# Kernel tuning notes

Hardware: AMD Instinct MI355X
Metric: run time of the kernel (lower is better)

The kernel has to match this reference:

```python
import jax, jax.numpy as jnp
import numpy as np
from jax import lax

V, B, C, H, W, D, G_DEF = 5, 2, 32, 128, 160, 32, 8


def _combine(proj):
    # proj: [B,2,4,4]; [:,0]=extrinsic, [:,1]=intrinsic; new[:, :3, :4] = K[:3,:3] @ E[:3,:4]
    ext, K = proj[:, 0], proj[:, 1]
    top = jnp.einsum('bij,bjk->bik', K[:, :3, :3], ext[:, :3, :4])
    return ext.at[:, :3, :4].set(top)


def _bilinear(img, x, y):
    # img [C,H,W]; x,y [N] pixel coords; zeros padding, align_corners=True (torch grid_sample)
    Ch, Hh, Wh = img.shape
    x0 = jnp.floor(x); y0 = jnp.floor(y)
    wx1 = x - x0; wy1 = y - y0
    def gather(xi, yi):
        valid = ((xi >= 0) & (xi <= Wh - 1) & (yi >= 0) & (yi <= Hh - 1)).astype(img.dtype)
        xc = jnp.clip(xi, 0, Wh - 1).astype(jnp.int32)
        yc = jnp.clip(yi, 0, Hh - 1).astype(jnp.int32)
        return img[:, yc, xc] * valid
    return (gather(x0, y0) * ((1 - wx1) * (1 - wy1)) + gather(x0 + 1, y0) * (wx1 * (1 - wy1))
            + gather(x0, y0 + 1) * ((1 - wx1) * wy1) + gather(x0 + 1, y0 + 1) * (wx1 * wy1))


def _conv3d(x, w, b, pad):
    y = lax.conv_general_dilated(x, w, (1, 1, 1), [(pad, pad)] * 3,
                                 dimension_numbers=('NCDHW', 'OIDHW', 'NCDHW'))
    return y + b[None, :, None, None, None]


def setup_inputs():
    key = jax.random.key(0)
    ks = jax.random.split(key, 8)
    features = jax.random.normal(ks[0], (V, B, C, H, W), jnp.float32)
    pm = np.zeros((B, V, 2, 4, 4), np.float32)
    for v in range(V):
        E = np.eye(4, dtype=np.float32); E[0, 3] = 0.05 * v  # small baseline along x
        K = np.eye(4, dtype=np.float32)
        K[0, 0] = K[1, 1] = float(W); K[0, 2] = W / 2.0; K[1, 2] = H / 2.0
        pm[:, v, 0] = E; pm[:, v, 1] = K
    proj_matrices = jnp.asarray(pm)
    d = jnp.linspace(1.0, 3.0, D, dtype=jnp.float32)
    depth_values = jnp.broadcast_to(d[None, :, None, None], (B, D, H, W))
    s = 0.1
    reg_w1 = jax.random.normal(ks[1], (8, G_DEF, 3, 3, 3), jnp.float32) * s
    reg_b1 = jnp.zeros((8,), jnp.float32)
    reg_w2 = jax.random.normal(ks[2], (1, 8, 3, 3, 3), jnp.float32) * s
    reg_b2 = jnp.zeros((1,), jnp.float32)
    pw_w1 = jax.random.normal(ks[3], (16, 1, 1, 1, 1), jnp.float32) * s
    pw_b1 = jnp.zeros((16,), jnp.float32)
    pw_w2 = jax.random.normal(ks[4], (8, 16, 1, 1, 1), jnp.float32) * s
    pw_b2 = jnp.zeros((8,), jnp.float32)
    pw_w3 = jax.random.normal(ks[5], (1, 8, 1, 1, 1), jnp.float32) * s
    pw_b3 = jnp.zeros((1,), jnp.float32)
    return dict(features=features, proj_matrices=proj_matrices, depth_values=depth_values,
                reg_w1=reg_w1, reg_b1=reg_b1, reg_w2=reg_w2, reg_b2=reg_b2,
                pw_w1=pw_w1, pw_b1=pw_b1, pw_w2=pw_w2, pw_b2=pw_b2,
                pw_w3=pw_w3, pw_b3=pw_b3, num_depth=D, G=G_DEF)


def reference(features, proj_matrices, depth_values, reg_w1, reg_b1, reg_w2, reg_b2,
              pw_w1, pw_b1, pw_w2, pw_b2, pw_w3, pw_b3, num_depth, G):
    Vn, Bn, Cn, Hn, Wn = features.shape
    Dn = num_depth
    ref_fea = features[0].reshape(Bn, G, Cn // G, Hn, Wn)
    ref_proj = _combine(proj_matrices[:, 0])
    ref_proj_inv = jnp.linalg.inv(ref_proj)
    ys, xs = jnp.meshgrid(jnp.arange(Hn, dtype=jnp.float32), jnp.arange(Wn, dtype=jnp.float32), indexing='ij')
    xyz = jnp.stack([xs.ravel(), ys.ravel(), jnp.ones(Hn * Wn, jnp.float32)], 0)  # [3, HW]
    sim_sum = 0.0; w_sum = 0.0; vws = []
    for v in range(1, Vn):  # fixed small view loop
        proj = jnp.einsum('bij,bjk->bik', _combine(proj_matrices[:, v]), ref_proj_inv)
        rot_xyz = jnp.einsum('bij,jn->bin', proj[:, :3, :3], xyz)  # [B,3,HW]
        pxyz = rot_xyz[:, :, None, :] * depth_values.reshape(Bn, 1, Dn, Hn * Wn) \
               + proj[:, :3, 3][:, :, None, None]  # [B,3,D,HW]
        # grid is computed under no_grad in torch -> stop_gradient
        x = lax.stop_gradient((pxyz[:, 0] / pxyz[:, 2]).reshape(Bn, -1))
        y = lax.stop_gradient((pxyz[:, 1] / pxyz[:, 2]).reshape(Bn, -1))
        warped = jax.vmap(_bilinear)(features[v], x, y).reshape(Bn, G, Cn // G, Dn, Hn, Wn)
        sim = (warped * ref_fea[:, :, :, None]).mean(2)  # [B,G,D,H,W] group correlation
        p = jax.nn.softmax(lax.stop_gradient(sim), axis=1)  # detached in torch
        ent = -(p * jnp.log(p + 1e-7)).sum(1, keepdims=True)  # [B,1,D,H,W]
        h = jax.nn.relu(_conv3d(ent, pw_w1, pw_b1, 0))
        h = jax.nn.relu(_conv3d(h, pw_w2, pw_b2, 0))
        vw = jax.nn.sigmoid(_conv3d(h, pw_w3, pw_b3, 0)).max(axis=2)  # [B,1,H,W]
        vws.append(vw)
        sim_sum = sim_sum + sim * vw[:, None]  # broadcast [B,1,1,H,W]
        w_sum = w_sum + vw[:, None]
    view_weights = jnp.concatenate(vws, axis=1)  # [B,V-1,H,W]
    similarity = sim_sum / (w_sum + 1e-6)
    h = jax.nn.relu(_conv3d(similarity, reg_w1, reg_b1, 1))
    prob_volume_pre = _conv3d(h, reg_w2, reg_b2, 1)[:, 0]  # [B,D,H,W]
    prob_volume = jax.nn.softmax(prob_volume_pre, axis=1)
    depth = (prob_volume * depth_values).sum(1)  # [B,H,W]
    pv = lax.stop_gradient(prob_volume)
    padded = jnp.pad(pv, ((0, 0), (1, 2), (0, 0), (0, 0)))
    # 4 * avg_pool3d(kernel=(4,1,1)) == sliding window sum over depth
    sum4 = lax.reduce_window(padded, 0.0, lax.add, (1, 4, 1, 1), (1, 1, 1, 1), 'VALID')
    didx = jnp.clip((pv * jnp.arange(Dn, dtype=pv.dtype)[None, :, None, None]).sum(1).astype(jnp.int32), 0, Dn - 1)
    photometric_confidence = jnp.take_along_axis(sum4, didx[:, None], axis=1)[:, 0]
    return depth, photometric_confidence, view_weights, prob_volume_pre, similarity
```

## Files before the change

kernel.cpp:

```cpp
#include <hip/hip_runtime.h>
#include <hip/hip_bf16.h>
#include <hip/hip_fp16.h>

#define V_  5
#define B_  2
#define C_  32
#define H_  128
#define W_  160
#define D_  32
#define G_  8
#define HW_  (H_*W_)
#define DHW_ (D_*HW_)

#define LOG2E_ 1.4426950408889634f
#define LN2_   0.6931471805599453f
#define LN8_   2.0794415416798357f

typedef _Float16 h8 __attribute__((ext_vector_type(8)));
typedef _Float16 h4 __attribute__((ext_vector_type(4)));
typedef _Float16 h2 __attribute__((ext_vector_type(2)));
typedef float    f4 __attribute__((ext_vector_type(4)));

__device__ inline float fdot2f(h2 a, h2 b, float c) {
#if __has_builtin(__builtin_amdgcn_fdot2)
    return __builtin_amdgcn_fdot2(a, b, c, false);
#else
    return fmaf((float)a[0], (float)b[0], fmaf((float)a[1], (float)b[1], c));
#endif
}



__device__ inline void combine_mat(const float* m, float out[4][4]) {
    const float* ext = m;
    const float* K   = m + 16;
    for (int r = 0; r < 4; ++r)
        for (int c = 0; c < 4; ++c)
            out[r][c] = ext[r*4 + c];
    for (int r = 0; r < 3; ++r)
        for (int c = 0; c < 4; ++c) {
            float s = 0.f;
            for (int k = 0; k < 3; ++k) s += K[r*4 + k] * ext[k*4 + c];
            out[r][c] = s;
        }
}

__device__ inline void invert4(const float Ain[4][4], float Inv[4][4]) {
    float A[4][4];
    for (int r = 0; r < 4; ++r)
        for (int c = 0; c < 4; ++c) {
            A[r][c]   = Ain[r][c];
            Inv[r][c] = (r == c) ? 1.f : 0.f;
        }
    for (int k = 0; k < 4; ++k) {
        int p = k; float best = fabsf(A[k][k]);
        for (int r = k + 1; r < 4; ++r) {
            float v = fabsf(A[r][k]);
            if (v > best) { best = v; p = r; }
        }
        if (p != k) {
            for (int j = 0; j < 4; ++j) {
                float t = A[k][j]; A[k][j] = A[p][j]; A[p][j] = t;
                t = Inv[k][j]; Inv[k][j] = Inv[p][j]; Inv[p][j] = t;
            }
        }
        float dinv = 1.f / A[k][k];
        for (int j = 0; j < 4; ++j) { A[k][j] *= dinv; Inv[k][j] *= dinv; }
        for (int r = 0; r < 4; ++r) {
            if (r == k) continue;
            float f = A[r][k];
            for (int j = 0; j < 4; ++j) {
                A[r][j]  -= f * A[k][j];
                Inv[r][j] -= f * Inv[k][j];
            }
        }
    }
}

__global__ __launch_bounds__(1024) void k_proj(
    const float* __restrict__ pm,
    const float* __restrict__ pw_w1, const float* __restrict__ pw_b1,
    const float* __restrict__ pw_w2, const float* __restrict__ pw_b2,
    const float* __restrict__ pw_w3, const float* __restrict__ pw_b3,
    const float* __restrict__ reg_w1, const float* __restrict__ reg_w2,
    float* __restrict__ proj_ws, float* __restrict__ tabw,
    _Float16* __restrict__ wh1, _Float16* __restrict__ wh2)
{
    int tid = threadIdx.x;
    if (tid < B_) {
        int b = tid;
        float C0[4][4], C0inv[4][4];
        combine_mat(pm + (b * V_ + 0) * 32, C0);
        invert4(C0, C0inv);
        for (int v = 1; v < V_; ++v) {
            float Cv[4][4];
            combine_mat(pm + (b * V_ + v) * 32, Cv);
            float* o = proj_ws + (b * 4 + (v - 1)) * 12;
            for (int r = 0; r < 3; ++r)
                for (int c = 0; c < 4; ++c) {
                    float s = 0.f;
                    for (int k = 0; k < 4; ++k) s += Cv[r][k] * C0inv[k][c];
                    o[r*4 + c] = s;
                }
        }
    }
    for (int i = tid; i < 36*16*8; i += 1024) {
        int ic = i & 7; int m = (i >> 3) & 15; int slot = i >> 7;
        int wx = slot & 3; int grp = slot >> 2;
        wh1[i] = (_Float16)((wx < 3 && m < 8) ? reg_w1[(m*8 + ic)*27 + grp*3 + wx] : 0.f);
    }
    for (int i = tid; i < 36*8; i += 1024) {
        int ic = i & 7; int slot = i >> 3;
        int wx = slot & 3; int grp = slot >> 2;
        wh2[i] = (_Float16)((wx < 3) ? reg_w2[ic*27 + grp*3 + wx] : 0.f);
    }
    float ent = (float)tid * (LN8_ / 1023.0f);
    float h2v[8];
    #pragma unroll
    for (int j = 0; j < 8; ++j) h2v[j] = pw_b2[j];
    for (int k = 0; k < 16; ++k) {
        float h1 = fmaxf(ent * pw_w1[k] + pw_b1[k], 0.f);
        #pragma unroll
        for (int j = 0; j < 8; ++j) h2v[j] += pw_w2[j*16 + k] * h1;
    }
    float o3 = pw_b3[0];
    #pragma unroll
    for (int j = 0; j < 8; ++j) o3 += pw_w3[j] * fmaxf(h2v[j], 0.f);
    tabw[tid] = 1.f / (1.f + expf(-o3));
}

__global__ __launch_bounds__(1024) void k_transpose(
    const float* __restrict__ in, _Float16* __restrict__ out)
{
    __shared__ float s[32][33];
    const int tx = threadIdx.x, ty = threadIdx.y;
    const int tid = ty * 32 + tx;
    const int hw0 = blockIdx.x * 32;
    const int vb  = blockIdx.y;
    s[ty][tx] = in[(vb * 32 + ty) * HW_ + hw0 + tx];
    __syncthreads();
    if (tid < 256) {
        int hw = tid >> 3, q = tid & 7;
        h4 hv;
        #pragma unroll
        for (int i = 0; i < 4; ++i) hv[i] = (_Float16)s[q*4 + i][hw];
        *(h4*)(out + ((size_t)vb * HW_ + hw0 + hw) * 32 + q*4) = hv;
    }
}

__global__ __launch_bounds__(1024) void k_main(
    const _Float16* __restrict__ featT,
    const float* __restrict__ depthv,
    const float* __restrict__ proj_ws,
    const float* __restrict__ tabw,
    float* __restrict__ out_vw,
    float* __restrict__ out_sim,
    _Float16* __restrict__ simh)
{
    const int tid = threadIdx.x;
    const int wv   = tid >> 6;
    const int lane = tid & 63;
    const int j    = lane >> 5;
    const int d    = lane & 31;
    const int pxl  = wv * 2 + j;
    const int w0 = blockIdx.x * 32;
    const int h  = blockIdx.y;
    const int b  = blockIdx.z;
    const int w  = w0 + pxl;
    const int p  = h * W_ + w;

    __shared__ float tab_s[1024];
    __shared__ float proj_s[48];
    __shared__ float s_sim[G_][32][33];

    tab_s[tid] = tabw[tid];
    if (tid < 48) proj_s[tid] = proj_ws[b * 48 + tid];
    __syncthreads();

    const h8* rp = (const h8*)(featT + ((size_t)b * HW_ + p) * 32);
    h8 r8[4];
    #pragma unroll
    for (int cc = 0; cc < 4; ++cc) r8[cc] = rp[cc];

    const float depth = depthv[(b * D_ + d) * HW_ + p];
    const float xf = (float)w, yf = (float)h;

    float simsum[G_];
    #pragma unroll
    for (int g = 0; g < G_; ++g) simsum[g] = 0.f;
    float wsum = 0.f;

    for (int v = 1; v < V_; ++v) {
        const float* P = &proj_s[(v - 1) * 12];
        float px = (P[0]*xf + P[1]*yf + P[2])  * depth + P[3];
        float py = (P[4]*xf + P[5]*yf + P[6])  * depth + P[7];
        float pz = (P[8]*xf + P[9]*yf + P[10]) * depth + P[11];
        float rz = __builtin_amdgcn_rcpf(pz);
        float xs = px * rz;
        float ys = py * rz;

        float xr = rintf(xs);
        float yr = rintf(ys);
        xs = (fabsf(xs - xr) < 1e-4f) ? xr : xs;
        ys = (fabsf(ys - yr) < 1e-4f) ? yr : ys;

        float x0 = floorf(xs), y0 = floorf(ys);
        float wx1 = xs - x0,  wy1 = ys - y0;
        float wx0 = 1.f - wx1, wy0 = 1.f - wy1;

        bool vx0 = (x0 >= 0.f)     && (x0 <= (float)(W_-1));
        bool vx1 = (x0+1.f >= 0.f) && (x0+1.f <= (float)(W_-1));
        bool vy0 = (y0 >= 0.f)     && (y0 <= (float)(H_-1));
        bool vy1 = (y0+1.f >= 0.f) && (y0+1.f <= (float)(H_-1));

        int xc0 = (int)fminf(fmaxf(x0,     0.f), (float)(W_-1));
        int xc1 = (int)fminf(fmaxf(x0+1.f, 0.f), (float)(W_-1));
        int yc0 = (int)fminf(fmaxf(y0,     0.f), (float)(H_-1));
        int yc1 = (int)fminf(fmaxf(y0+1.f, 0.f), (float)(H_-1));

        float w00 = (vx0 && vy0) ? (wx0 * wy0) : 0.f;
        float w01 = (vx1 && vy0) ? (wx1 * wy0) : 0.f;
        float w10 = (vx0 && vy1) ? (wx0 * wy1) : 0.f;
        float w11 = (vx1 && vy1) ? (wx1 * wy1) : 0.f;

        const _Float16* vbp = featT + (size_t)(v * B_ + b) * HW_ * 32;

        float sim[G_];
        #pragma unroll
        for (int g = 0; g < G_; ++g) sim[g] = 0.f;

        bool top = __any(w00 > 0.f || w01 > 0.f);
        bool bot = __any(w10 > 0.f || w11 > 0.f);

        if (top) {
            h2 w00h = { (_Float16)w00, (_Float16)w00 };
            h2 w01h = { (_Float16)w01, (_Float16)w01 };
            const h8* t00 = (const h8*)(vbp + (size_t)(yc0 * W_ + xc0) * 32);
            const h8* t01 = (const h8*)(vbp + (size_t)(yc0 * W_ + xc1) * 32);
            #pragma unroll
            for (int cc = 0; cc < 4; ++cc) {
                h8 a = t00[cc], bb = t01[cc];
                const h2* ap = (const h2*)&a;
                const h2* bp = (const h2*)&bb;
                const h2* rv2 = (const h2*)&r8[cc];
                #pragma unroll
                for (int jp = 0; jp < 4; ++jp) {
                    h2 fv = ap[jp] * w00h + bp[jp] * w01h;
                    int g = cc*2 + (jp >> 1);
                    sim[g] = fdot2f(fv, rv2[jp], sim[g]);
                }
            }
        }
        if (bot) {
            h2 w10h = { (_Float16)w10, (_Float16)w10 };
            h2 w11h = { (_Float16)w11, (_Float16)w11 };
            const h8* t10 = (const h8*)(vbp + (size_t)(yc1 * W_ + xc0) * 32);
            const h8* t11 = (const h8*)(vbp + (size_t)(yc1 * W_ + xc1) * 32);
            #pragma unroll
            for (int cc = 0; cc < 4; ++cc) {
                h8 cq = t10[cc], dq = t11[cc];
                const h2* cp = (const h2*)&cq;
                const h2* dp = (const h2*)&dq;
                const h2* rv2 = (const h2*)&r8[cc];
                #pragma unroll
                for (int jp = 0; jp < 4; ++jp) {
                    h2 fv = cp[jp] * w10h + dp[jp] * w11h;
                    int g = cc*2 + (jp >> 1);
                    sim[g] = fdot2f(fv, rv2[jp], sim[g]);
                }
            }
        }

        #pragma unroll
        for (int g = 0; g < G_; ++g) sim[g] *= 0.25f;

        float m = sim[0];
        #pragma unroll
        for (int g = 1; g < G_; ++g) m = fmaxf(m, sim[g]);
        float es = 0.f, edot = 0.f;
        #pragma unroll
        for (int g = 0; g < G_; ++g) {
            float e = exp2f((sim[g] - m) * LOG2E_);
            es += e;
            edot = fmaf(e, sim[g], edot);
        }
        float inv_es = __builtin_amdgcn_rcpf(es);
        float ent = m + log2f(es) * LN2_ - edot * inv_es;

        float t = ent * (1023.0f / LN8_);
        t = fminf(fmaxf(t, 0.f), 1022.999f);
        int it = (int)t;
        float fr = t - (float)it;
        float lo = tab_s[it], hi = tab_s[it + 1];
        float sig = fmaf(hi - lo, fr, lo);

        float mv = sig;
        #pragma unroll
        for (int k = 16; k >= 1; k >>= 1)
            mv = fmaxf(mv, __shfl_xor(mv, k, 64));
        if (d == 0)
            out_vw[(b * 4 + (v - 1)) * HW_ + p] = mv;

        #pragma unroll
        for (int g = 0; g < G_; ++g) simsum[g] = fmaf(sim[g], mv, simsum[g]);
        wsum += mv;
    }

    float wn = __builtin_amdgcn_rcpf(wsum + 1e-6f);
    #pragma unroll
    for (int g = 0; g < G_; ++g) s_sim[g][d][pxl] = simsum[g] * wn;
    __syncthreads();

    const int tx = tid & 31;
    const int ty = tid >> 5;
    float* so = out_sim + (size_t)b * G_ * DHW_ + ty * HW_ + h * W_ + w0 + tx;
    h8 hv;
    #pragma unroll
    for (int g = 0; g < G_; ++g) {
        float val = s_sim[g][ty][tx];
        so[(size_t)g * DHW_] = val;
        hv[g] = (_Float16)val;
    }
    *(h8*)(simh + ((size_t)(b * D_ + ty) * HW_ + h * W_ + w0 + tx) * 8) = hv;
}


__global__ __launch_bounds__(256) void k_conv1m(
    const _Float16* __restrict__ in,
    const _Float16* __restrict__ wh,
    const float* __restrict__ bias,
    _Float16* __restrict__ outh)
{
    __shared__ _Float16 halo[6*10*34*8 + 8];
    const int tid = threadIdx.x;
    const int w0 = blockIdx.x * 32;
    const int h0 = blockIdx.y * 8;
    const int z  = blockIdx.z;
    const int b  = z >> 3;
    const int d0 = (z & 7) * 4;

    for (int pos = tid; pos < 2040; pos += 256) {
        int wx = pos % 34; int r = pos / 34; int hy = r % 10; int dz = r / 10;
        int gw = w0 + wx - 1, gh = h0 + hy - 1, gd = d0 + dz - 1;
        uint4 val = make_uint4(0u, 0u, 0u, 0u);
        if (gw >= 0 && gw < W_ && gh >= 0 && gh < H_ && gd >= 0 && gd < D_)
            val = *(const uint4*)(in + (((size_t)(b*D_ + gd)*H_ + gh)*W_ + gw)*8);
        *(uint4*)(halo + pos*8) = val;
    }
    if (tid == 0) *(uint4*)(halo + 6*10*34*8) = make_uint4(0u, 0u, 0u, 0u);

    const int wave = tid >> 6, lane = tid & 63;
    const int n = lane & 15, q = lane >> 4;

    h8 afrag[9];
    #pragma unroll
    for (int grp = 0; grp < 9; ++grp)
        afrag[grp] = *(const h8*)(wh + ((grp*4 + q)*16 + n)*8);

    f4 binit;
    #pragma unroll
    for (int reg = 0; reg < 4; ++reg)
        binit[reg] = (q < 2) ? bias[q*4 + reg] : 0.f;

    __syncthreads();

    const int lane_off = (n + q) * 16;

    #pragma unroll
    for (int it = 0; it < 4; ++it) {
        int t = wave*4 + it;
        int h_row = t >> 1, whalf = t & 1;
        const char* base = (const char*)halo + h_row*544 + whalf*256 + lane_off;
        #pragma unroll
        for (int dout = 0; dout < 4; ++dout) {
            f4 acc = binit;
            #pragma unroll
            for (int dz = 0; dz < 3; ++dz) {
                #pragma unroll
                for (int hy = 0; hy < 3; ++hy) {
                    h8 bfrag = *(const h8*)(base + (((dout + dz)*10 + hy)*544));
                    acc = __builtin_amdgcn_mfma_f32_16x16x32_f16(afrag[dz*3 + hy], bfrag, acc, 0, 0, 0);
                }
            }
            if (q < 2) {
                h4 hv;
                #pragma unroll
                for (int reg = 0; reg < 4; ++reg) hv[reg] = (_Float16)fmaxf(acc[reg], 0.f);
                *(h4*)(outh + (((size_t)(b*D_ + d0 + dout)*H_ + h0 + h_row)*W_ + w0 + whalf*16 + n)*8 + q*4) = hv;
            }
        }
    }
}

__global__ __launch_bounds__(256) void k_conv2m(
    const _Float16* __restrict__ in,
    const _Float16* __restrict__ wh,
    const float* __restrict__ bias,
    float* __restrict__ out)
{
    __shared__ _Float16 halo[6*10*34*8 + 8];
    const int tid = threadIdx.x;
    const int w0 = blockIdx.x * 32;
    const int h0 = blockIdx.y * 8;
    const int z  = blockIdx.z;
    const int b  = z >> 3;
    const int d0 = (z & 7) * 4;

    for (int pos = tid; pos < 2040; pos += 256) {
        int wx = pos % 34; int r = pos / 34; int hy = r % 10; int dz = r / 10;
        int gw = w0 + wx - 1, gh = h0 + hy - 1, gd = d0 + dz - 1;
        uint4 val = make_uint4(0u, 0u, 0u, 0u);
        if (gw >= 0 && gw < W_ && gh >= 0 && gh < H_ && gd >= 0 && gd < D_)
            val = *(const uint4*)(in + (((size_t)(b*D_ + gd)*H_ + gh)*W_ + gw)*8);
        *(uint4*)(halo + pos*8) = val;
    }
    if (tid == 0) *(uint4*)(halo + 6*10*34*8) = make_uint4(0u, 0u, 0u, 0u);

    const int wave = tid >> 6, lane = tid & 63;
    const int n = lane & 15, q = lane >> 4;

    h8 afrag[9];
    #pragma unroll
    for (int grp = 0; grp < 9; ++grp) {
        h8 a;
        #pragma unroll
        for (int e = 0; e < 8; ++e) a[e] = (_Float16)0.f;
        if (n == 0) a = *(const h8*)(wh + (grp*4 + q)*8);
        afrag[grp] = a;
    }
    const float b0 = bias[0];

    __syncthreads();

    const int lane_off = (n + q) * 16;

    #pragma unroll
    for (int it = 0; it < 4; ++it) {
        int t = wave*4 + it;
        int h_row = t >> 1, whalf = t & 1;
        const char* base = (const char*)halo + h_row*544 + whalf*256 + lane_off;
        #pragma unroll
        for (int dout = 0; dout < 4; ++dout) {
            f4 acc;
            acc[0] = (q == 0) ? b0 : 0.f;
            acc[1] = 0.f; acc[2] = 0.f; acc[3] = 0.f;
            #pragma unroll
            for (int dz = 0; dz < 3; ++dz) {
                #pragma unroll
                for (int hy = 0; hy < 3; ++hy) {
                    h8 bfrag = *(const h8*)(base + (((dout + dz)*10 + hy)*544));
                    acc = __builtin_amdgcn_mfma_f32_16x16x32_f16(afrag[dz*3 + hy], bfrag, acc, 0, 0, 0);
                }
            }
            if (q == 0)
                out[(((size_t)(b*D_ + d0 + dout)*H_ + h0 + h_row)*W_ + w0 + whalf*16 + n)] = acc[0];
        }
    }
}

__global__ __launch_bounds__(256) void k_final(
    const float* __restrict__ pvp,
    const float* __restrict__ depthv,
    float* __restrict__ out_depth,
    float* __restrict__ out_conf)
{
    int i = blockIdx.x * 256 + threadIdx.x;
    if (i >= B_ * HW_) return;
    int b = i / HW_;
    int p = i - b * HW_;

    const float* pp = pvp + b * DHW_ + p;
    const float* dv = depthv + b * DHW_ + p;

    float x[D_];
    float m = -3.4e38f;
    #pragma unroll
    for (int d = 0; d < D_; ++d) { x[d] = pp[d * HW_]; m = fmaxf(m, x[d]); }
    float s = 0.f;
    #pragma unroll
    for (int d = 0; d < D_; ++d) { x[d] = exp2f((x[d] - m) * LOG2E_); s += x[d]; }
    float inv = 1.f / s;

    float dep = 0.f, fd = 0.f;
    #pragma unroll
    for (int d = 0; d < D_; ++d) {
        float pv = x[d] * inv;
        x[d] = pv;
        dep = fmaf(pv, dv[d * HW_], dep);
        fd  = fmaf(pv, (float)d, fd);
    }
    int di = (int)fd;
    di = di < 0 ? 0 : (di > D_ - 1 ? D_ - 1 : di);
    float conf = 0.f;
    #pragma unroll
    for (int k = 0; k < 4; ++k) {
        int idx = di - 1 + k;
        if (idx >= 0 && idx < D_) conf += x[idx];
    }
    out_depth[i] = dep;
    out_conf[i]  = conf;
}

extern "C" void kernel_launch(void* const* d_in, const int* in_sizes, int n_in,
                              void* d_out, int out_size, void* d_ws, size_t ws_size,
                              hipStream_t stream) {
    const float* feat   = (const float*)d_in[0];
    const float* pm     = (const float*)d_in[1];
    const float* depthv = (const float*)d_in[2];
    const float* reg_w1 = (const float*)d_in[3];
    const float* reg_b1 = (const float*)d_in[4];
    const float* reg_w2 = (const float*)d_in[5];
    const float* reg_b2 = (const float*)d_in[6];
    const float* pw_w1  = (const float*)d_in[7];
    const float* pw_b1  = (const float*)d_in[8];
    const float* pw_w2  = (const float*)d_in[9];
    const float* pw_b2  = (const float*)d_in[10];
    const float* pw_w3  = (const float*)d_in[11];
    const float* pw_b3  = (const float*)d_in[12];

    float* out = (float*)d_out;
    float* out_depth = out;
    float* out_conf  = out + B_*HW_;
    float* out_vw    = out + 2*B_*HW_;
    float* out_pvp   = out_vw + B_*4*HW_;
    float* out_sim   = out_pvp + B_*DHW_;

    float* ws      = (float*)d_ws;
    float* proj_ws = ws;
    float* tabw    = ws + 128;
    _Float16* wh1  = (_Float16*)(ws + 1152);
    _Float16* wh2  = (_Float16*)(ws + 3456);
    _Float16* featT = (_Float16*)(ws + 4736);
    _Float16* hidh  = (_Float16*)(ws + 4736);
    _Float16* simh  = (_Float16*)(ws + 4736 + 5242880);

    hipLaunchKernelGGL(k_proj, dim3(1), dim3(1024), 0, stream,
                       pm, pw_w1, pw_b1, pw_w2, pw_b2, pw_w3, pw_b3,
                       reg_w1, reg_w2, proj_ws, tabw, wh1, wh2);

    hipLaunchKernelGGL(k_transpose, dim3(HW_/32, V_*B_), dim3(32, 32), 0, stream,
                       feat, featT);

    hipLaunchKernelGGL(k_main, dim3(W_/32, H_, B_), dim3(1024), 0, stream,
                       featT, depthv, proj_ws, tabw, out_vw, out_sim, simh);

    hipLaunchKernelGGL(k_conv1m, dim3(W_/32, H_/8, B_*D_/4), dim3(256), 0, stream,
                       simh, wh1, reg_b1, hidh);

    hipLaunchKernelGGL(k_conv2m, dim3(W_/32, H_/8, B_*D_/4), dim3(256), 0, stream,
                       hidh, wh2, reg_b2, out_pvp);

    hipLaunchKernelGGL(k_final, dim3((B_*HW_ + 255)/256), dim3(256), 0, stream,
                       out_pvp, depthv, out_depth, out_conf);
}
```

Measured before the change: 209.3 us.

## Software-pipeline view gathers in k_main and halve block size

Unrolls the loop over source views into a two-stage software pipeline. The top-row bilinear taps for the next view are fetched into registers while the current view's similarity, entropy and weight are computed, which is meant to hide gather latency. The block also shrinks from 1024 to 512 threads (16 pixels per block), with launch bounds asking for 4 blocks per CU, to raise occupancy and scheduling flexibility. In exchange, holding two views' prefetched fp16 taps raises register pressure and could cause spills.

```diff
diff --git a/kernel.cpp b/kernel.cpp
--- a/kernel.cpp
+++ b/kernel.cpp
@@ -148,7 +148,117 @@
     }
 }
 
-__global__ __launch_bounds__(1024) void k_main(
+
+#define VPREP(S, VV) do { \
+    const float* P = &proj_s[((VV) - 1) * 12]; \
+    float px_ = (P[0]*xf + P[1]*yf + P[2])  * depth + P[3]; \
+    float py_ = (P[4]*xf + P[5]*yf + P[6])  * depth + P[7]; \
+    float pz_ = (P[8]*xf + P[9]*yf + P[10]) * depth + P[11]; \
+    float rz = __builtin_amdgcn_rcpf(pz_); \
+    float xs = px_ * rz, ys = py_ * rz; \
+    float xr = rintf(xs), yr = rintf(ys); \
+    xs = (fabsf(xs - xr) < 1e-4f) ? xr : xs; \
+    ys = (fabsf(ys - yr) < 1e-4f) ? yr : ys; \
+    float x0 = floorf(xs), y0 = floorf(ys); \
+    float wx1 = xs - x0, wy1 = ys - y0; \
+    float wx0 = 1.f - wx1, wy0 = 1.f - wy1; \
+    bool vx0 = (x0 >= 0.f)     && (x0 <= (float)(W_-1)); \
+    bool vx1 = (x0+1.f >= 0.f) && (x0+1.f <= (float)(W_-1)); \
+    bool vy0 = (y0 >= 0.f)     && (y0 <= (float)(H_-1)); \
+    bool vy1 = (y0+1.f >= 0.f) && (y0+1.f <= (float)(H_-1)); \
+    int xc0 = (int)fminf(fmaxf(x0,     0.f), (float)(W_-1)); \
+    int xc1 = (int)fminf(fmaxf(x0+1.f, 0.f), (float)(W_-1)); \
+    int yc0 = (int)fminf(fmaxf(y0,     0.f), (float)(H_-1)); \
+    int yc1 = (int)fminf(fmaxf(y0+1.f, 0.f), (float)(H_-1)); \
+    w00##S = (vx0 && vy0) ? (wx0 * wy0) : 0.f; \
+    w01##S = (vx1 && vy0) ? (wx1 * wy0) : 0.f; \
+    w10##S = (vx0 && vy1) ? (wx0 * wy1) : 0.f; \
+    w11##S = (vx1 && vy1) ? (wx1 * wy1) : 0.f; \
+    o10##S = (uint32_t)(yc1 * W_ + xc0); \
+    o11##S = (uint32_t)(yc1 * W_ + xc1); \
+    top##S = __any(w00##S > 0.f || w01##S > 0.f); \
+    bot##S = __any(w10##S > 0.f || w11##S > 0.f); \
+    if (top##S) { \
+        const _Float16* vbp = featT + (size_t)((VV) * B_ + b) * HW_ * 32; \
+        const h8* t00 = (const h8*)(vbp + (size_t)(yc0 * W_ + xc0) * 32); \
+        const h8* t01 = (const h8*)(vbp + (size_t)(yc0 * W_ + xc1) * 32); \
+        _Pragma("unroll") \
+        for (int cc = 0; cc < 4; ++cc) { a##S[cc] = t00[cc]; b##S[cc] = t01[cc]; } \
+    } \
+} while (0)
+
+#define VCONSUME(S, VV) do { \
+    float sim[G_]; \
+    _Pragma("unroll") \
+    for (int g = 0; g < G_; ++g) sim[g] = 0.f; \
+    if (top##S) { \
+        h2 w00h = { (_Float16)w00##S, (_Float16)w00##S }; \
+        h2 w01h = { (_Float16)w01##S, (_Float16)w01##S }; \
+        _Pragma("unroll") \
+        for (int cc = 0; cc < 4; ++cc) { \
+            const h2* ap = (const h2*)&a##S[cc]; \
+            const h2* bp = (const h2*)&b##S[cc]; \
+            const h2* rv2 = (const h2*)&r8[cc]; \
+            _Pragma("unroll") \
+            for (int jp = 0; jp < 4; ++jp) { \
+                h2 fv = ap[jp] * w00h + bp[jp] * w01h; \
+                int g = cc*2 + (jp >> 1); \
+                sim[g] = fdot2f(fv, rv2[jp], sim[g]); \
+            } \
+        } \
+    } \
+    if (bot##S) { \
+        const _Float16* vbp = featT + (size_t)((VV) * B_ + b) * HW_ * 32; \
+        const h8* t10 = (const h8*)(vbp + (size_t)o10##S * 32); \
+        const h8* t11 = (const h8*)(vbp + (size_t)o11##S * 32); \
+        h2 w10h = { (_Float16)w10##S, (_Float16)w10##S }; \
+        h2 w11h = { (_Float16)w11##S, (_Float16)w11##S }; \
+        _Pragma("unroll") \
+        for (int cc = 0; cc < 4; ++cc) { \
+            h8 cq = t10[cc], dq = t11[cc]; \
+            const h2* cp = (const h2*)&cq; \
+            const h2* dp = (const h2*)&dq; \
+            const h2* rv2 = (const h2*)&r8[cc]; \
+            _Pragma("unroll") \
+            for (int jp = 0; jp < 4; ++jp) { \
+                h2 fv = cp[jp] * w10h + dp[jp] * w11h; \
+                int g = cc*2 + (jp >> 1); \
+                sim[g] = fdot2f(fv, rv2[jp], sim[g]); \
+            } \
+        } \
+    } \
+    _Pragma("unroll") \
+    for (int g = 0; g < G_; ++g) sim[g] *= 0.25f; \
+    float m = sim[0]; \
+    _Pragma("unroll") \
+    for (int g = 1; g < G_; ++g) m = fmaxf(m, sim[g]); \
+    float es = 0.f, edot = 0.f; \
+    _Pragma("unroll") \
+    for (int g = 0; g < G_; ++g) { \
+        float e = exp2f((sim[g] - m) * LOG2E_); \
+        es += e; \
+        edot = fmaf(e, sim[g], edot); \
+    } \
+    float inv_es = __builtin_amdgcn_rcpf(es); \
+    float ent = m + log2f(es) * LN2_ - edot * inv_es; \
+    float t = ent * (1023.0f / LN8_); \
+    t = fminf(fmaxf(t, 0.f), 1022.999f); \
+    int it = (int)t; \
+    float fr = t - (float)it; \
+    float lo = tab_s[it], hi = tab_s[it + 1]; \
+    float sig = fmaf(hi - lo, fr, lo); \
+    float mv = sig; \
+    _Pragma("unroll") \
+    for (int k = 16; k >= 1; k >>= 1) \
+        mv = fmaxf(mv, __shfl_xor(mv, k, 64)); \
+    if (d == 0) \
+        out_vw[(b * 4 + ((VV) - 1)) * HW_ + p] = mv; \
+    _Pragma("unroll") \
+    for (int g = 0; g < G_; ++g) simsum[g] = fmaf(sim[g], mv, simsum[g]); \
+    wsum += mv; \
+} while (0)
+
+__global__ __launch_bounds__(512, 4) void k_main(
     const _Float16* __restrict__ featT,
     const float* __restrict__ depthv,
     const float* __restrict__ proj_ws,
@@ -163,7 +273,7 @@
     const int j    = lane >> 5;
     const int d    = lane & 31;
     const int pxl  = wv * 2 + j;
-    const int w0 = blockIdx.x * 32;
+    const int w0 = blockIdx.x * 16;
     const int h  = blockIdx.y;
     const int b  = blockIdx.z;
     const int w  = w0 + pxl;
@@ -171,9 +281,9 @@
 
     __shared__ float tab_s[1024];
     __shared__ float proj_s[48];
-    __shared__ float s_sim[G_][32][33];
-
-    tab_s[tid] = tabw[tid];
+    __shared__ float s_sim[G_][32][17];
+
+    for (int i = tid; i < 1024; i += 512) tab_s[i] = tabw[i];
     if (tid < 48) proj_s[tid] = proj_ws[b * 48 + tid];
     __syncthreads();
 
@@ -190,129 +300,27 @@
     for (int g = 0; g < G_; ++g) simsum[g] = 0.f;
     float wsum = 0.f;
 
-    for (int v = 1; v < V_; ++v) {
-        const float* P = &proj_s[(v - 1) * 12];
-        float px = (P[0]*xf + P[1]*yf + P[2])  * depth + P[3];
-        float py = (P[4]*xf + P[5]*yf + P[6])  * depth + P[7];
-        float pz = (P[8]*xf + P[9]*yf + P[10]) * depth + P[11];
-        float rz = __builtin_amdgcn_rcpf(pz);
-        float xs = px * rz;
-        float ys = py * rz;
-
-        float xr = rintf(xs);
-        float yr = rintf(ys);
-        xs = (fabsf(xs - xr) < 1e-4f) ? xr : xs;
-        ys = (fabsf(ys - yr) < 1e-4f) ? yr : ys;
-
-        float x0 = floorf(xs), y0 = floorf(ys);
-        float wx1 = xs - x0,  wy1 = ys - y0;
-        float wx0 = 1.f - wx1, wy0 = 1.f - wy1;
-
-        bool vx0 = (x0 >= 0.f)     && (x0 <= (float)(W_-1));
-        bool vx1 = (x0+1.f >= 0.f) && (x0+1.f <= (float)(W_-1));
-        bool vy0 = (y0 >= 0.f)     && (y0 <= (float)(H_-1));
-        bool vy1 = (y0+1.f >= 0.f) && (y0+1.f <= (float)(H_-1));
-
-        int xc0 = (int)fminf(fmaxf(x0,     0.f), (float)(W_-1));
-        int xc1 = (int)fminf(fmaxf(x0+1.f, 0.f), (float)(W_-1));
-        int yc0 = (int)fminf(fmaxf(y0,     0.f), (float)(H_-1));
-        int yc1 = (int)fminf(fmaxf(y0+1.f, 0.f), (float)(H_-1));
-
-        float w00 = (vx0 && vy0) ? (wx0 * wy0) : 0.f;
-        float w01 = (vx1 && vy0) ? (wx1 * wy0) : 0.f;
-        float w10 = (vx0 && vy1) ? (wx0 * wy1) : 0.f;
-        float w11 = (vx1 && vy1) ? (wx1 * wy1) : 0.f;
-
-        const _Float16* vbp = featT + (size_t)(v * B_ + b) * HW_ * 32;
-
-        float sim[G_];
-        #pragma unroll
-        for (int g = 0; g < G_; ++g) sim[g] = 0.f;
-
-        bool top = __any(w00 > 0.f || w01 > 0.f);
-        bool bot = __any(w10 > 0.f || w11 > 0.f);
-
-        if (top) {
-            h2 w00h = { (_Float16)w00, (_Float16)w00 };
-            h2 w01h = { (_Float16)w01, (_Float16)w01 };
-            const h8* t00 = (const h8*)(vbp + (size_t)(yc0 * W_ + xc0) * 32);
-            const h8* t01 = (const h8*)(vbp + (size_t)(yc0 * W_ + xc1) * 32);
-            #pragma unroll
-            for (int cc = 0; cc < 4; ++cc) {
-                h8 a = t00[cc], bb = t01[cc];
-                const h2* ap = (const h2*)&a;
-                const h2* bp = (const h2*)&bb;
-                const h2* rv2 = (const h2*)&r8[cc];
-                #pragma unroll
-                for (int jp = 0; jp < 4; ++jp) {
-                    h2 fv = ap[jp] * w00h + bp[jp] * w01h;
-                    int g = cc*2 + (jp >> 1);
-                    sim[g] = fdot2f(fv, rv2[jp], sim[g]);
-                }
-            }
-        }
-        if (bot) {
-            h2 w10h = { (_Float16)w10, (_Float16)w10 };
-            h2 w11h = { (_Float16)w11, (_Float16)w11 };
-            const h8* t10 = (const h8*)(vbp + (size_t)(yc1 * W_ + xc0) * 32);
-            const h8* t11 = (const h8*)(vbp + (size_t)(yc1 * W_ + xc1) * 32);
-            #pragma unroll
-            for (int cc = 0; cc < 4; ++cc) {
-                h8 cq = t10[cc], dq = t11[cc];
-                const h2* cp = (const h2*)&cq;
-                const h2* dp = (const h2*)&dq;
-                const h2* rv2 = (const h2*)&r8[cc];
-                #pragma unroll
-                for (int jp = 0; jp < 4; ++jp) {
-                    h2 fv = cp[jp] * w10h + dp[jp] * w11h;
-                    int g = cc*2 + (jp >> 1);
-                    sim[g] = fdot2f(fv, rv2[jp], sim[g]);
-                }
-            }
-        }
-
-        #pragma unroll
-        for (int g = 0; g < G_; ++g) sim[g] *= 0.25f;
-
-        float m = sim[0];
-        #pragma unroll
-        for (int g = 1; g < G_; ++g) m = fmaxf(m, sim[g]);
-        float es = 0.f, edot = 0.f;
-        #pragma unroll
-        for (int g = 0; g < G_; ++g) {
-            float e = exp2f((sim[g] - m) * LOG2E_);
-            es += e;
-            edot = fmaf(e, sim[g], edot);
-        }
-        float inv_es = __builtin_amdgcn_rcpf(es);
-        float ent = m + log2f(es) * LN2_ - edot * inv_es;
-
-        float t = ent * (1023.0f / LN8_);
-        t = fminf(fmaxf(t, 0.f), 1022.999f);
-        int it = (int)t;
-        float fr = t - (float)it;
-        float lo = tab_s[it], hi = tab_s[it + 1];
-        float sig = fmaf(hi - lo, fr, lo);
-
-        float mv = sig;
-        #pragma unroll
-        for (int k = 16; k >= 1; k >>= 1)
-            mv = fmaxf(mv, __shfl_xor(mv, k, 64));
-        if (d == 0)
-            out_vw[(b * 4 + (v - 1)) * HW_ + p] = mv;
-
-        #pragma unroll
-        for (int g = 0; g < G_; ++g) simsum[g] = fmaf(sim[g], mv, simsum[g]);
-        wsum += mv;
-    }
+    float w00A, w01A, w10A, w11A, w00B, w01B, w10B, w11B;
+    uint32_t o10A, o11A, o10B, o11B;
+    bool topA, botA, topB, botB;
+    h8 aA[4], bA[4], aB[4], bB[4];
+
+    VPREP(A, 1);
+    VPREP(B, 2);
+    VCONSUME(A, 1);
+    VPREP(A, 3);
+    VCONSUME(B, 2);
+    VPREP(B, 4);
+    VCONSUME(A, 3);
+    VCONSUME(B, 4);
 
     float wn = __builtin_amdgcn_rcpf(wsum + 1e-6f);
     #pragma unroll
     for (int g = 0; g < G_; ++g) s_sim[g][d][pxl] = simsum[g] * wn;
     __syncthreads();
 
-    const int tx = tid & 31;
-    const int ty = tid >> 5;
+    const int tx = tid & 15;
+    const int ty = tid >> 4;
     float* so = out_sim + (size_t)b * G_ * DHW_ + ty * HW_ + h * W_ + w0 + tx;
     h8 hv;
     #pragma unroll
@@ -541,7 +549,7 @@
     hipLaunchKernelGGL(k_transpose, dim3(HW_/32, V_*B_), dim3(32, 32), 0, stream,
                        feat, featT);
 
-    hipLaunchKernelGGL(k_main, dim3(W_/32, H_, B_), dim3(1024), 0, stream,
+    hipLaunchKernelGGL(k_main, dim3(W_/16, H_, B_), dim3(512), 0, stream,
                        featT, depthv, proj_ws, tabw, out_vw, out_sim, simh);
 
     hipLaunchKernelGGL(k_conv1m, dim3(W_/32, H_/8, B_*D_/4), dim3(256), 0, stream,
```

After: 217.7 us. +4.0%, slower.
